# Optimization experiments

Hardware: AMD Instinct MI355X
Metric: run time of the kernel (lower is better)

## Reference

```python
import jax, jax.numpy as jnp
import numpy as np

NEG_INF = -1e9


def setup_inputs() -> dict:
    key = jax.random.key(0)
    ks = jax.random.split(key, 9)
    B, T, E, D, H = 64, 2048, 1024, 1024, 1024
    enc = jax.random.normal(ks[0], (B, T, E), dtype=jnp.float32)
    dec = jax.random.normal(ks[1], (B, D), dtype=jnp.float32)
    inp_mask = jax.random.randint(ks[2], (B, T), 0, 2, dtype=jnp.int32)
    s = 1.0 / np.sqrt(H)
    W_enc = jax.random.normal(ks[3], (E, H), dtype=jnp.float32) * s
    b_enc = jax.random.normal(ks[4], (H,), dtype=jnp.float32) * 0.01
    W_dec = jax.random.normal(ks[5], (D, H), dtype=jnp.float32) * s
    b_dec = jax.random.normal(ks[6], (H,), dtype=jnp.float32) * 0.01
    W_out = jax.random.normal(ks[7], (H, 1), dtype=jnp.float32) * s
    b_out = jax.random.normal(ks[8], (1,), dtype=jnp.float32) * 0.01
    return {"enc": enc, "dec": dec, "inp_mask": inp_mask,
            "W_enc": W_enc, "b_enc": b_enc, "W_dec": W_dec, "b_dec": b_dec,
            "W_out": W_out, "b_out": b_out}


def reference(enc, dec, inp_mask, W_enc, b_enc, W_dec, b_dec, W_out, b_out):
    # a: [B, T, H] = Linear(enc) + Linear(dec)[:, None, :]
    a = jnp.einsum('bte,eh->bth', enc, W_enc) + b_enc \
        + (dec @ W_dec + b_dec)[:, None, :]
    a = jnp.tanh(a)
    # scores: [B, T]
    scores = (jnp.einsum('bth,h->bt', a, W_out[:, 0]) + b_out[0])
    scores = jnp.where(inp_mask == 0, NEG_INF, scores)
    probs = jax.nn.softmax(scores, axis=1)            # [B, T]
    attn = jnp.einsum('bt,bte->be', probs, enc)       # [B, E]
    return (attn, probs)
```

## Files before the change

### kernel.cpp

```cpp
#include <hip/hip_runtime.h>
#include <hip/hip_bf16.h>

typedef __attribute__((ext_vector_type(4))) float f32x4;
typedef __attribute__((ext_vector_type(4))) unsigned int u32x4;
typedef __attribute__((ext_vector_type(2))) unsigned int u32x2;
typedef __attribute__((ext_vector_type(8))) short s16x8;

static constexpr int Bb = 64;
static constexpr int Tt = 2048;
static constexpr int Ee = 1024;
static constexpr int Hh = 1024;
static constexpr int ATTN_N = Bb * Ee;
static constexpr int PROB_N = Bb * Tt;

__device__ inline unsigned short f2bf(float f) {
    __hip_bfloat16 h = __float2bfloat16(f);
    return __builtin_bit_cast(unsigned short, h);
}
__device__ inline float bf2f(unsigned short u) {
    return __builtin_bit_cast(float, (unsigned)u << 16);
}

__device__ inline void gload_lds16(const unsigned short* g, unsigned short* l) {
    __builtin_amdgcn_global_load_lds(
        (const __attribute__((address_space(1))) void*)g,
        (__attribute__((address_space(3))) void*)l,
        16, 0, 0);
}

__global__ void wtrans_kernel(const float* __restrict__ w_enc,
                              unsigned short* __restrict__ w16t) {
    __shared__ float tile[32][33];
    const int bx = blockIdx.x & 31;
    const int by = blockIdx.x >> 5;
    const int tx = threadIdx.x & 31;
    const int ty = threadIdx.x >> 5;
#pragma unroll
    for (int j = 0; j < 4; ++j) {
        int e = by * 32 + ty + j * 8;
        int h = bx * 32 + tx;
        tile[ty + j * 8][tx] = w_enc[e * Hh + h];
    }
    __syncthreads();
#pragma unroll
    for (int j = 0; j < 4; ++j) {
        int h = bx * 32 + ty + j * 8;
        int e = by * 32 + tx;
        w16t[h * Ee + e] = f2bf(tile[tx][ty + j * 8]);
    }
}

__global__ void ddec_kernel(const float* __restrict__ dec,
                            const float* __restrict__ w_dec,
                            const float* __restrict__ b_dec,
                            const float* __restrict__ b_enc,
                            float* __restrict__ ddec) {
    const int b = blockIdx.y;
    const int h = blockIdx.x * 256 + threadIdx.x;
    float acc = b_dec[h] + b_enc[h];
    const float* dr = dec + b * Ee;
#pragma unroll 4
    for (int e = 0; e < Ee; ++e) {
        acc += dr[e] * w_dec[e * Hh + h];
    }
    ddec[b * Hh + h] = acc;
}

__global__ __launch_bounds__(256) void e2bf_kernel(const float* __restrict__ src,
                                                   unsigned short* __restrict__ dst,
                                                   long long n8) {
    long long i = (long long)blockIdx.x * 256 + threadIdx.x;
    const long long stride = (long long)gridDim.x * 256;
    for (; i < n8; i += stride) {
        const f32x4* s = reinterpret_cast<const f32x4*>(src + i * 8);
        f32x4 a = s[0], b = s[1];
        u32x4 w;
        w.x = (unsigned)f2bf(a.x) | ((unsigned)f2bf(a.y) << 16);
        w.y = (unsigned)f2bf(a.z) | ((unsigned)f2bf(a.w) << 16);
        w.z = (unsigned)f2bf(b.x) | ((unsigned)f2bf(b.y) << 16);
        w.w = (unsigned)f2bf(b.z) | ((unsigned)f2bf(b.w) << 16);
        *reinterpret_cast<u32x4*>(dst + i * 8) = w;
    }
}

__global__ __launch_bounds__(512, 1) void gemm_score_bf16a(
    const unsigned short* __restrict__ a16, const unsigned short* __restrict__ w16t,
    const float* __restrict__ ddec, const float* __restrict__ w_out,
    float* __restrict__ scores) {
    __shared__ unsigned short As[2][256 * 64];
    __shared__ unsigned short Bs[2][256 * 64];

    const int tid = threadIdx.x;
    const int lane = tid & 63;
    const int wid = tid >> 6;
    const int wm = wid >> 2;
    const int wn = wid & 3;
    const int lr = lane & 15;
    const int lg = lane >> 4;

    const int g = blockIdx.x;
    const int xcd = g & 7;
    const int slot = g >> 3;
    const int ntile = slot & 3;
    const int mtile = xcd * 64 + (slot >> 2);
    const int m0 = mtile * 256;
    const int n0 = ntile * 256;
    const int bidx = m0 >> 11;

    const int sg = (lane & 7) ^ (lane >> 3);
    auto stageA = [&](int kt, int db) {
#pragma unroll
        for (int c = 0; c < 4; ++c) {
            int rr = (wid * 4 + c) * 8 + (lane >> 3);
            const unsigned short* src = a16 + (size_t)(m0 + rr) * Ee + kt * 64 + sg * 8;
            gload_lds16(src, &As[db][(wid * 4 + c) * 512]);
        }
    };
    auto stageB = [&](int kt, int db) {
#pragma unroll
        for (int c = 0; c < 4; ++c) {
            int rr = (wid * 4 + c) * 8 + (lane >> 3);
            const unsigned short* src = w16t + (size_t)(n0 + rr) * Ee + kt * 64 + sg * 8;
            gload_lds16(src, &Bs[db][(wid * 4 + c) * 512]);
        }
    };

    f32x4 acc[8][4];
#pragma unroll
    for (int ni = 0; ni < 4; ++ni) {
        float dv = ddec[bidx * Hh + n0 + wn * 64 + ni * 16 + lr];
#pragma unroll
        for (int mi = 0; mi < 8; ++mi) {
            acc[mi][ni].x = dv; acc[mi][ni].y = dv;
            acc[mi][ni].z = dv; acc[mi][ni].w = dv;
        }
    }

    u32x4 af[4], bf[4];
    auto readB4 = [&](int db, int kh) {
        const char* bbase = (const char*)&Bs[db][0];
        const int kb = kh * 64 + lg * 16;
#pragma unroll
        for (int ni = 0; ni < 4; ++ni) {
            int r = wn * 64 + ni * 16 + lr;
            bf[ni] = *reinterpret_cast<const u32x4*>(bbase + r * 128 + (kb ^ ((r & 7) << 4)));
        }
    };
    auto readA4 = [&](int db, int kh, int mib) {
        const char* abase = (const char*)&As[db][0];
        const int kb = kh * 64 + lg * 16;
#pragma unroll
        for (int k = 0; k < 4; ++k) {
            int r = wm * 128 + (mib + k) * 16 + lr;
            af[k] = *reinterpret_cast<const u32x4*>(abase + r * 128 + (kb ^ ((r & 7) << 4)));
        }
    };
    auto mfma16 = [&](int mib) {
        __builtin_amdgcn_s_setprio(1);
#pragma unroll
        for (int k = 0; k < 4; ++k)
#pragma unroll
            for (int ni = 0; ni < 4; ++ni)
                acc[mib + k][ni] = __builtin_amdgcn_mfma_f32_16x16x32_bf16(
                    __builtin_bit_cast(s16x8, af[k]),
                    __builtin_bit_cast(s16x8, bf[ni]),
                    acc[mib + k][ni], 0, 0, 0);
        __builtin_amdgcn_s_setprio(0);
    };

#define BARRIER() do { asm volatile("" ::: "memory"); \
    __builtin_amdgcn_s_barrier(); asm volatile("" ::: "memory"); } while (0)
#define LGKM0() asm volatile("s_waitcnt lgkmcnt(0)" ::: "memory")

    stageA(0, 0);
    stageB(0, 0);
    asm volatile("s_waitcnt vmcnt(0)" ::: "memory");
    BARRIER();

#pragma unroll 1
    for (int tt = 0; tt < 16; tt += 2) {
#pragma unroll
        for (int p = 0; p < 2; ++p) {
            const int t = tt + p;
            readB4(p, 0);
            readA4(p, 0, 0);
            if (t < 15) { stageA(t + 1, p ^ 1); stageB(t + 1, p ^ 1); }
            BARRIER(); LGKM0();
            mfma16(0);
            BARRIER();
            readA4(p, 0, 4);
            BARRIER(); LGKM0();
            mfma16(4);
            BARRIER();
            readB4(p, 1);
            readA4(p, 1, 0);
            BARRIER(); LGKM0();
            mfma16(0);
            BARRIER();
            readA4(p, 1, 4);
            if (t < 15) asm volatile("s_waitcnt vmcnt(0)" ::: "memory");
            BARRIER(); LGKM0();
            mfma16(4);
            BARRIER();
        }
    }

    float wout[4];
#pragma unroll
    for (int ni = 0; ni < 4; ++ni)
        wout[ni] = w_out[n0 + wn * 64 + ni * 16 + lr];

#pragma unroll
    for (int mi = 0; mi < 8; ++mi) {
#pragma unroll
        for (int i = 0; i < 4; ++i) {
            float s = 0.f;
#pragma unroll
            for (int ni = 0; ni < 4; ++ni) {
                float x = (i == 0) ? acc[mi][ni].x : (i == 1) ? acc[mi][ni].y
                           : (i == 2) ? acc[mi][ni].z : acc[mi][ni].w;
                float t = 1.f - 2.f / (__expf(2.f * x) + 1.f);
                s += t * wout[ni];
            }
            s += __shfl_xor(s, 1);
            s += __shfl_xor(s, 2);
            s += __shfl_xor(s, 4);
            s += __shfl_xor(s, 8);
            if (lr == 0) {
                int row = m0 + wm * 128 + mi * 16 + 4 * lg + i;
                atomicAdd(&scores[row], s);
            }
        }
    }
#undef BARRIER
#undef LGKM0
}

__global__ __launch_bounds__(512, 1) void gemm_score_kernel(
    const float* __restrict__ enc, const unsigned short* __restrict__ w16t,
    const float* __restrict__ ddec, const float* __restrict__ w_out,
    float* __restrict__ scores) {
    __shared__ unsigned short As[2][256 * 64];
    __shared__ unsigned short Bs[2][256 * 64];

    const int tid = threadIdx.x;
    const int lane = tid & 63;
    const int wid = tid >> 6;
    const int wm = wid >> 2;
    const int wn = wid & 3;
    const int lr = lane & 15;
    const int lg = lane >> 4;

    const int g = blockIdx.x;
    const int xcd = g & 7;
    const int slot = g >> 3;
    const int ntile = slot & 3;
    const int mtile = xcd * 64 + (slot >> 2);
    const int m0 = mtile * 256;
    const int n0 = ntile * 256;
    const int bidx = m0 >> 11;

    const int ar = tid >> 3;
    const int as = tid & 7;

    f32x4 rs[8];

    auto loadA = [&](int kt) {
        const float* src = enc + (size_t)(m0 + ar) * Ee + kt * 64 + as * 8;
#pragma unroll
        for (int ci = 0; ci < 4; ++ci) {
            rs[ci * 2]     = *reinterpret_cast<const f32x4*>(src + (size_t)(64 * ci) * Ee);
            rs[ci * 2 + 1] = *reinterpret_cast<const f32x4*>(src + (size_t)(64 * ci) * Ee + 4);
        }
    };
    auto writeA = [&](int db) {
        char* abase = (char*)&As[db][0];
#pragma unroll
        for (int ci = 0; ci < 4; ++ci) {
            int r = ar + 64 * ci;
            u32x4 w;
            w.x = (unsigned)f2bf(rs[2 * ci].x) | ((unsigned)f2bf(rs[2 * ci].y) << 16);
            w.y = (unsigned)f2bf(rs[2 * ci].z) | ((unsigned)f2bf(rs[2 * ci].w) << 16);
            w.z = (unsigned)f2bf(rs[2 * ci + 1].x) | ((unsigned)f2bf(rs[2 * ci + 1].y) << 16);
            w.w = (unsigned)f2bf(rs[2 * ci + 1].z) | ((unsigned)f2bf(rs[2 * ci + 1].w) << 16);
            *reinterpret_cast<u32x4*>(abase + r * 128 + ((as * 16) ^ ((r & 7) << 4))) = w;
        }
    };
    auto stageB = [&](int kt, int db) {
        const int sg = (lane & 7) ^ (lane >> 3);
#pragma unroll
        for (int c = 0; c < 4; ++c) {
            int rr = (wid * 4 + c) * 8 + (lane >> 3);
            const unsigned short* src = w16t + (size_t)(n0 + rr) * Ee + kt * 64 + sg * 8;
            gload_lds16(src, &Bs[db][(wid * 4 + c) * 512]);
        }
    };

    f32x4 acc[8][4];
#pragma unroll
    for (int ni = 0; ni < 4; ++ni) {
        float dv = ddec[bidx * Hh + n0 + wn * 64 + ni * 16 + lr];
#pragma unroll
        for (int mi = 0; mi < 8; ++mi) {
            acc[mi][ni].x = dv; acc[mi][ni].y = dv;
            acc[mi][ni].z = dv; acc[mi][ni].w = dv;
        }
    }

    u32x4 af[4], bf[4];
    auto readB4 = [&](int db, int kh) {
        const char* bbase = (const char*)&Bs[db][0];
        const int kb = kh * 64 + lg * 16;
#pragma unroll
        for (int ni = 0; ni < 4; ++ni) {
            int r = wn * 64 + ni * 16 + lr;
            bf[ni] = *reinterpret_cast<const u32x4*>(bbase + r * 128 + (kb ^ ((r & 7) << 4)));
        }
    };
    auto readA4 = [&](int db, int kh, int mib) {
        const char* abase = (const char*)&As[db][0];
        const int kb = kh * 64 + lg * 16;
#pragma unroll
        for (int k = 0; k < 4; ++k) {
            int r = wm * 128 + (mib + k) * 16 + lr;
            af[k] = *reinterpret_cast<const u32x4*>(abase + r * 128 + (kb ^ ((r & 7) << 4)));
        }
    };
    auto mfma16 = [&](int mib) {
        __builtin_amdgcn_s_setprio(1);
#pragma unroll
        for (int k = 0; k < 4; ++k)
#pragma unroll
            for (int ni = 0; ni < 4; ++ni)
                acc[mib + k][ni] = __builtin_amdgcn_mfma_f32_16x16x32_bf16(
                    __builtin_bit_cast(s16x8, af[k]),
                    __builtin_bit_cast(s16x8, bf[ni]),
                    acc[mib + k][ni], 0, 0, 0);
        __builtin_amdgcn_s_setprio(0);
    };

#define BARRIER() do { asm volatile("" ::: "memory"); \
    __builtin_amdgcn_s_barrier(); asm volatile("" ::: "memory"); } while (0)
#define LGKM0() asm volatile("s_waitcnt lgkmcnt(0)" ::: "memory")

    loadA(0);
    writeA(0);
    LGKM0();
    stageB(0, 0);
    loadA(1);
    asm volatile("s_waitcnt vmcnt(8)" ::: "memory");
    BARRIER();

#pragma unroll 1
    for (int t = 0; t < 16; ++t) {
        const int p = t & 1;
        readB4(p, 0);
        readA4(p, 0, 0);
        if (t < 15) stageB(t + 1, p ^ 1);
        BARRIER(); LGKM0();
        mfma16(0);
        BARRIER();
        readA4(p, 0, 4);
        BARRIER(); LGKM0();
        mfma16(4);
        BARRIER();
        readB4(p, 1);
        readA4(p, 1, 0);
        BARRIER(); LGKM0();
        mfma16(0);
        BARRIER();
        readA4(p, 1, 4);
        if (t < 15) writeA(p ^ 1);
        BARRIER(); LGKM0();
        if (t < 14) {
            loadA(t + 2);
            asm volatile("s_waitcnt vmcnt(8)" ::: "memory");
        } else if (t == 14) {
            asm volatile("s_waitcnt vmcnt(0)" ::: "memory");
        }
        mfma16(4);
        BARRIER();
    }

    float wout[4];
#pragma unroll
    for (int ni = 0; ni < 4; ++ni)
        wout[ni] = w_out[n0 + wn * 64 + ni * 16 + lr];

#pragma unroll
    for (int mi = 0; mi < 8; ++mi) {
#pragma unroll
        for (int i = 0; i < 4; ++i) {
            float s = 0.f;
#pragma unroll
            for (int ni = 0; ni < 4; ++ni) {
                float x = (i == 0) ? acc[mi][ni].x : (i == 1) ? acc[mi][ni].y
                           : (i == 2) ? acc[mi][ni].z : acc[mi][ni].w;
                float t = 1.f - 2.f / (__expf(2.f * x) + 1.f);
                s += t * wout[ni];
            }
            s += __shfl_xor(s, 1);
            s += __shfl_xor(s, 2);
            s += __shfl_xor(s, 4);
            s += __shfl_xor(s, 8);
            if (lr == 0) {
                int row = m0 + wm * 128 + mi * 16 + 4 * lg + i;
                atomicAdd(&scores[row], s);
            }
        }
    }
#undef BARRIER
#undef LGKM0
}

__global__ __launch_bounds__(256) void softmax_kernel(float* __restrict__ sc,
                                                      const int* __restrict__ mask) {
    __shared__ float red[256];
    const int b = blockIdx.x;
    const int tid = threadIdx.x;
    float* row = sc + b * Tt;
    const int* mrow = mask + b * Tt;

    float v[8];
    float mx = -3.0e38f;
#pragma unroll
    for (int j = 0; j < 8; ++j) {
        int t = tid + j * 256;
        float s = row[t];
        v[j] = (mrow[t] == 0) ? -1.0e9f : s;
        mx = fmaxf(mx, v[j]);
    }
    red[tid] = mx;
    __syncthreads();
    for (int off = 128; off > 0; off >>= 1) {
        if (tid < off) red[tid] = fmaxf(red[tid], red[tid + off]);
        __syncthreads();
    }
    mx = red[0];
    __syncthreads();

    float p[8];
    float sum = 0.f;
#pragma unroll
    for (int j = 0; j < 8; ++j) {
        p[j] = __expf(v[j] - mx);
        sum += p[j];
    }
    red[tid] = sum;
    __syncthreads();
    for (int off = 128; off > 0; off >>= 1) {
        if (tid < off) red[tid] += red[tid + off];
        __syncthreads();
    }
    float inv = 1.f / red[0];
#pragma unroll
    for (int j = 0; j < 8; ++j)
        row[tid + j * 256] = p[j] * inv;
}

__global__ __launch_bounds__(256) void attn_kernel(const float* __restrict__ enc,
                                                   const float* __restrict__ probs,
                                                   float* __restrict__ attn) {
    __shared__ float pr[128];
    const int b = blockIdx.y;
    const int tc = blockIdx.x;
    const int tid = threadIdx.x;
    if (tid < 128) pr[tid] = probs[b * Tt + tc * 128 + tid];
    __syncthreads();

    const int e0 = tid * 4;
    f32x4 acc; acc.x = 0.f; acc.y = 0.f; acc.z = 0.f; acc.w = 0.f;
    const float* base = enc + (size_t)b * Tt * Ee + (size_t)tc * 128 * Ee + e0;
#pragma unroll 4
    for (int t = 0; t < 128; ++t) {
        f32x4 vv = *reinterpret_cast<const f32x4*>(base + (size_t)t * Ee);
        float pw = pr[t];
        acc.x += pw * vv.x; acc.y += pw * vv.y;
        acc.z += pw * vv.z; acc.w += pw * vv.w;
    }
    atomicAdd(&attn[b * Ee + e0 + 0], acc.x);
    atomicAdd(&attn[b * Ee + e0 + 1], acc.y);
    atomicAdd(&attn[b * Ee + e0 + 2], acc.z);
    atomicAdd(&attn[b * Ee + e0 + 3], acc.w);
}

__global__ __launch_bounds__(256) void attn_kernel_bf16(
    const unsigned short* __restrict__ enc16,
    const float* __restrict__ probs, float* __restrict__ attn) {
    __shared__ float pr[128];
    const int b = blockIdx.y;
    const int tc = blockIdx.x;
    const int tid = threadIdx.x;
    if (tid < 128) pr[tid] = probs[b * Tt + tc * 128 + tid];
    __syncthreads();

    const int e0 = tid * 4;
    f32x4 acc; acc.x = 0.f; acc.y = 0.f; acc.z = 0.f; acc.w = 0.f;
    const unsigned short* base = enc16 + (size_t)b * Tt * Ee + (size_t)tc * 128 * Ee + e0;
#pragma unroll 4
    for (int t = 0; t < 128; ++t) {
        u32x2 w = *reinterpret_cast<const u32x2*>(base + (size_t)t * Ee);
        float pw = pr[t];
        acc.x += pw * bf2f((unsigned short)(w.x & 0xffff));
        acc.y += pw * bf2f((unsigned short)(w.x >> 16));
        acc.z += pw * bf2f((unsigned short)(w.y & 0xffff));
        acc.w += pw * bf2f((unsigned short)(w.y >> 16));
    }
    atomicAdd(&attn[b * Ee + e0 + 0], acc.x);
    atomicAdd(&attn[b * Ee + e0 + 1], acc.y);
    atomicAdd(&attn[b * Ee + e0 + 2], acc.z);
    atomicAdd(&attn[b * Ee + e0 + 3], acc.w);
}

extern "C" void kernel_launch(void* const* d_in, const int* in_sizes, int n_in,
                              void* d_out, int out_size, void* d_ws, size_t ws_size,
                              hipStream_t stream) {
    const float* enc      = (const float*)d_in[0];
    const float* dec      = (const float*)d_in[1];
    const int*   inp_mask = (const int*)d_in[2];
    const float* W_enc    = (const float*)d_in[3];
    const float* b_enc    = (const float*)d_in[4];
    const float* W_dec    = (const float*)d_in[5];
    const float* b_dec    = (const float*)d_in[6];
    const float* W_out    = (const float*)d_in[7];

    float* attn   = (float*)d_out;
    float* scores = (float*)d_out + ATTN_N;

    unsigned short* w16t = (unsigned short*)d_ws;
    const size_t W16T_BYTES = (size_t)Hh * Ee * 2;
    const size_t ENC16_BYTES = (size_t)Bb * Tt * Ee * 2;
    const bool fast = ws_size >= W16T_BYTES + ENC16_BYTES;
    unsigned short* enc16 = (unsigned short*)((char*)d_ws + W16T_BYTES);

    float* ddec = attn;

    hipMemsetAsync(scores, 0, (size_t)PROB_N * sizeof(float), stream);

    wtrans_kernel<<<dim3(1024), 256, 0, stream>>>(W_enc, w16t);
    ddec_kernel<<<dim3(4, 64), 256, 0, stream>>>(dec, W_dec, b_dec, b_enc, ddec);

    if (fast) {
        e2bf_kernel<<<dim3(2048), 256, 0, stream>>>(
            enc, enc16, (long long)Bb * Tt * Ee / 8);
        gemm_score_bf16a<<<dim3(2048), 512, 0, stream>>>(
            enc16, w16t, ddec, W_out, scores);
    } else {
        gemm_score_kernel<<<dim3(2048), 512, 0, stream>>>(
            enc, w16t, ddec, W_out, scores);
    }

    hipMemsetAsync(attn, 0, (size_t)ATTN_N * sizeof(float), stream);

    softmax_kernel<<<dim3(64), 256, 0, stream>>>(scores, inp_mask);
    if (fast) {
        attn_kernel_bf16<<<dim3(16, 64), 256, 0, stream>>>(enc16, scores, attn);
    } else {
        attn_kernel<<<dim3(16, 64), 256, 0, stream>>>(enc, scores, attn);
    }
}
```

Before: 735.4 us.

## Restructure GEMM main loop with two-tile-ahead prefetch and fewer barriers

Reorganizes the LDS double-buffered GEMM loop so each half-K step reads all A and B fragments at once and issues 32 MFMAs back to back, cutting barriers from eight to two per tile. Global-to-LDS staging now runs two tiles ahead into the buffer just consumed, and a partial vmcnt wait lets loads stay in flight across iterations. This is meant to remove barrier stalls and expose more memory latency hiding. In exchange it uses more registers for A fragments and depends on the vmcnt(8) count matching the number of outstanding loads.

```diff
diff --git a/kernel.cpp b/kernel.cpp
--- a/kernel.cpp
+++ b/kernel.cpp
@@ -136,8 +136,9 @@
         }
     }
 
-    u32x4 af[4], bf[4];
-    auto readB4 = [&](int db, int kh) {
+    u32x4 af[8], bf[4];
+    auto readKh = [&](int db, int kh) {
+        const char* abase = (const char*)&As[db][0];
         const char* bbase = (const char*)&Bs[db][0];
         const int kb = kh * 64 + lg * 16;
 #pragma unroll
@@ -145,26 +146,22 @@
             int r = wn * 64 + ni * 16 + lr;
             bf[ni] = *reinterpret_cast<const u32x4*>(bbase + r * 128 + (kb ^ ((r & 7) << 4)));
         }
-    };
-    auto readA4 = [&](int db, int kh, int mib) {
-        const char* abase = (const char*)&As[db][0];
-        const int kb = kh * 64 + lg * 16;
-#pragma unroll
-        for (int k = 0; k < 4; ++k) {
-            int r = wm * 128 + (mib + k) * 16 + lr;
+#pragma unroll
+        for (int k = 0; k < 8; ++k) {
+            int r = wm * 128 + k * 16 + lr;
             af[k] = *reinterpret_cast<const u32x4*>(abase + r * 128 + (kb ^ ((r & 7) << 4)));
         }
     };
-    auto mfma16 = [&](int mib) {
+    auto mfma32 = [&]() {
         __builtin_amdgcn_s_setprio(1);
 #pragma unroll
-        for (int k = 0; k < 4; ++k)
+        for (int k = 0; k < 8; ++k)
 #pragma unroll
             for (int ni = 0; ni < 4; ++ni)
-                acc[mib + k][ni] = __builtin_amdgcn_mfma_f32_16x16x32_bf16(
+                acc[k][ni] = __builtin_amdgcn_mfma_f32_16x16x32_bf16(
                     __builtin_bit_cast(s16x8, af[k]),
                     __builtin_bit_cast(s16x8, bf[ni]),
-                    acc[mib + k][ni], 0, 0, 0);
+                    acc[k][ni], 0, 0, 0);
         __builtin_amdgcn_s_setprio(0);
     };
 
@@ -176,31 +173,27 @@
     stageB(0, 0);
     asm volatile("s_waitcnt vmcnt(0)" ::: "memory");
     BARRIER();
+    stageA(1, 1);
+    stageB(1, 1);
 
 #pragma unroll 1
     for (int tt = 0; tt < 16; tt += 2) {
 #pragma unroll
         for (int p = 0; p < 2; ++p) {
             const int t = tt + p;
-            readB4(p, 0);
-            readA4(p, 0, 0);
-            if (t < 15) { stageA(t + 1, p ^ 1); stageB(t + 1, p ^ 1); }
-            BARRIER(); LGKM0();
-            mfma16(0);
+            readKh(p, 0);
+            mfma32();
+            readKh(p, 1);
+            LGKM0();
             BARRIER();
-            readA4(p, 0, 4);
-            BARRIER(); LGKM0();
-            mfma16(4);
-            BARRIER();
-            readB4(p, 1);
-            readA4(p, 1, 0);
-            BARRIER(); LGKM0();
-            mfma16(0);
-            BARRIER();
-            readA4(p, 1, 4);
-            if (t < 15) asm volatile("s_waitcnt vmcnt(0)" ::: "memory");
-            BARRIER(); LGKM0();
-            mfma16(4);
+            if (t < 14) {
+                stageA(t + 2, p);
+                stageB(t + 2, p);
+                asm volatile("s_waitcnt vmcnt(8)" ::: "memory");
+            } else if (t == 14) {
+                asm volatile("s_waitcnt vmcnt(0)" ::: "memory");
+            }
+            mfma32();
             BARRIER();
         }
     }
```

New measurement: 1.166 ms. 58.6% more time.
